# Kernel tuning notes

Measured on AMD Instinct MI355X. Metric: run time of the kernel, lower is better.

Reference implementation:

```python
import jax, jax.numpy as jnp
import numpy as np

B, N, F_IN = 8, 4096, 32
NRP = 1024
D_MODEL = 512
K = 64  # max_num_neighbors
STAGE_CFG = ((1024, 0.05), (256, 0.3), (64, 0.5))  # (num_samples=ceil(0.25*N_in), radius)


def fps(pos, m):
    """Farthest point sampling of m points from pos (N,3), deterministic start at 0."""
    d = jnp.sum((pos - pos[0]) ** 2, axis=-1)
    idxs = jnp.zeros((m,), jnp.int32)
    def body(i, carry):
        idxs, d = carry
        nxt = jnp.argmax(d).astype(jnp.int32)
        d = jnp.minimum(d, jnp.sum((pos - pos[nxt]) ** 2, axis=-1))
        return (idxs.at[i].set(nxt), d)
    idxs, _ = jax.lax.fori_loop(1, m, body, (idxs, d))
    return idxs


def apply_mlp(h, ws, bs):
    for w, b in zip(ws[:-1], bs[:-1]):
        h = jax.nn.relu(h @ w + b)
    return h @ ws[-1] + bs[-1]


def sa_stage(x, pos, m, r, ws, bs):
    """SAModule: FPS -> radius neighbors (<=K) -> PointNetConv (gather, MLP, max-scatter)."""
    idx = jax.vmap(lambda p: fps(p, m))(pos)                          # (B,m)
    pos_s = jnp.take_along_axis(pos, idx[..., None], axis=1)          # (B,m,3)
    d2 = jnp.sum((pos_s[:, :, None, :] - pos[:, None, :, :]) ** 2, -1)  # (B,m,N)
    neg = jnp.where(d2 <= r * r, -d2, -jnp.inf)
    vals, nbr = jax.lax.top_k(neg, K)                                 # (B,m,K) nearest within r
    valid = vals > -jnp.inf                                           # self always valid (d2=0)
    x_j = jax.vmap(lambda xb, nb: xb[nb])(x, nbr)                     # (B,m,K,F) gather
    p_j = jax.vmap(lambda pb, nb: pb[nb])(pos, nbr)                   # (B,m,K,3)
    h = jnp.concatenate([x_j, p_j - pos_s[:, :, None, :]], axis=-1)   # message input
    h = apply_mlp(h, ws, bs)
    h = jnp.where(valid[..., None], h, -jnp.inf)
    return jnp.max(h, axis=2), pos_s                                  # max aggregation


def _forward(point_cloud_features, point_cloud, emb_table, point_id_emb, stage_params):
    x = emb_table[point_cloud_features[..., 0]]                       # (B,N,F_IN)
    x = x.at[:, :NRP].add(point_id_emb)
    pos = point_cloud
    for (m, r), (ws, bs) in zip(STAGE_CFG, stage_params):
        x, pos = sa_stage(x, pos, m, r, ws, bs)
    return x, pos                                                     # (B,64,D_MODEL), (B,64,3)


def setup_inputs() -> dict:
    key = jax.random.key(0)
    ks = iter(jax.random.split(key, 64))
    def nrm(shape, s=0.05):
        return s * jax.random.normal(next(ks), shape, dtype=jnp.float32)
    inp = {
        "point_cloud_features": jax.random.randint(next(ks), (B, N, 1), 0, 3),
        "point_cloud": jax.random.uniform(next(ks), (B, N, 3), dtype=jnp.float32),
        "emb_table": nrm((3, F_IN), 1.0),
        "point_id_emb": nrm((1, NRP, F_IN), 1.0),
    }
    dims = {"s1": [3 + F_IN, 64, 64, 64], "s2": [64 + 3, 128, 128, 256], "s3": [256 + 3, 256, 512, D_MODEL]}
    for s, d in dims.items():
        for i in range(3):
            inp[f"{s}w{i}"] = nrm((d[i], d[i + 1]))
            inp[f"{s}b{i}"] = jnp.zeros((d[i + 1],), jnp.float32)
    return inp


def reference(point_cloud_features, point_cloud, emb_table, point_id_emb,
              s1w0, s1b0, s1w1, s1b1, s1w2, s1b2,
              s2w0, s2b0, s2w1, s2b1, s2w2, s2b2,
              s3w0, s3b0, s3w1, s3b1, s3w2, s3b2):
    stage_params = [
        ([s1w0, s1w1, s1w2], [s1b0, s1b1, s1b2]),
        ([s2w0, s2w1, s2w2], [s2b0, s2b1, s2b2]),
        ([s3w0, s3w1, s3w2], [s3b0, s3b1, s3b2]),
    ]
    return _forward(point_cloud_features, point_cloud, emb_table, point_id_emb, stage_params)
```

## Files before the change

kernel.cpp:

```cpp
#include <hip/hip_runtime.h>

#define DEVI static __device__ __forceinline__

constexpr int B = 8;
constexpr int N0 = 4096;
constexpr int KNB = 64;

typedef float f32x2 __attribute__((ext_vector_type(2)));
typedef float f32x4 __attribute__((ext_vector_type(4)));
typedef short bf16x8 __attribute__((ext_vector_type(8)));

DEVI float dist2f(float ax, float ay, float az, float bx, float by, float bz) {
#pragma clang fp contract(off)
  float dx = ax - bx;
  float dy = ay - by;
  float dz = az - bz;
  return (dx * dx + dy * dy) + dz * dz;
}
DEVI f32x2 dist2v(f32x2 ax, f32x2 ay, f32x2 az, float bx, float by, float bz) {
#pragma clang fp contract(off)
  f32x2 dx = ax - bx;
  f32x2 dy = ay - by;
  f32x2 dz = az - bz;
  return (dx * dx + dy * dy) + dz * dz;
}

DEVI unsigned long long packMinKey(float v, int i) {
  return ((unsigned long long)__float_as_uint(v) << 32) | (unsigned int)i;
}

template <int CTRL, int RM>
DEVI float dppMaxF32(float v) {
  int o = __builtin_amdgcn_update_dpp(__float_as_int(v), __float_as_int(v),
                                      CTRL, RM, 0xf, false);
  return fmaxf(v, __int_as_float(o));
}
DEVI float waveMaxF32(float v) {
  v = dppMaxF32<0x111, 0xf>(v);
  v = dppMaxF32<0x112, 0xf>(v);
  v = dppMaxF32<0x114, 0xf>(v);
  v = dppMaxF32<0x118, 0xf>(v);
  v = dppMaxF32<0x142, 0xa>(v);
  v = dppMaxF32<0x143, 0xc>(v);
  return __int_as_float(__builtin_amdgcn_readlane(__float_as_int(v), 63));
}
template <int CTRL, int RM>
DEVI unsigned dppMinU32(unsigned v) {
  int o = __builtin_amdgcn_update_dpp((int)v, (int)v, CTRL, RM, 0xf, false);
  unsigned ov = (unsigned)o;
  return v < ov ? v : ov;
}
DEVI unsigned waveMinU32(unsigned v) {
  v = dppMinU32<0x111, 0xf>(v);
  v = dppMinU32<0x112, 0xf>(v);
  v = dppMinU32<0x114, 0xf>(v);
  v = dppMinU32<0x118, 0xf>(v);
  v = dppMinU32<0x142, 0xa>(v);
  v = dppMinU32<0x143, 0xc>(v);
  return (unsigned)__builtin_amdgcn_readlane((int)v, 63);
}

DEVI unsigned short bfhi(float x) {
  unsigned u = __float_as_uint(x);
  return (unsigned short)((u + 0x7FFFu + ((u >> 16) & 1u)) >> 16);
}
DEVI float bf2f(unsigned short h) { return __uint_as_float(((unsigned)h) << 16); }
DEVI void mkfrag(const float* p, bf16x8& hi, bf16x8& lo) {
#pragma unroll
  for (int e = 0; e < 8; ++e) {
    float x = p[e];
    unsigned short h = bfhi(x);
    float r = x - bf2f(h);
    unsigned short l2 = bfhi(r);
    hi[e] = (short)h;
    lo[e] = (short)l2;
  }
}


DEVI void x0_body(const int* __restrict__ feat, const float* __restrict__ emb,
                  const float* __restrict__ pid, float* __restrict__ x0buf,
                  int bx, int t) {
  int gid = bx * 256 + t;
  if (gid >= B * N0 * 32) return;
  int c = gid & 31;
  int bn = gid >> 5;
  int n = bn & (N0 - 1);
  int f = feat[bn];
  float v = emb[f * 32 + c];
  if (n < 1024) v += pid[n * 32 + c];
  x0buf[gid] = v;
}

template <int NPTS, int M, int BLK>
DEVI void fps_body(char* smem, const float* __restrict__ pos,
                   float* __restrict__ pos_out, int b, int t) {
  constexpr int EPT = NPTS / BLK;
  constexpr int EP2 = EPT / 2;
  constexpr int NW = BLK / 64;
  float4* posl = (float4*)smem;
  float4* outp = (float4*)(smem + (size_t)NPTS * 16);
  unsigned long long* redk =
      (unsigned long long*)(smem + (size_t)(NPTS + M) * 16);
  const float* pb = pos + (size_t)b * NPTS * 3;
  f32x2 px[EP2], py[EP2], pz[EP2], d[EP2];
#pragma unroll
  for (int e = 0; e < EP2; ++e) {
    int i0 = t + (2 * e) * BLK;
    int i1 = t + (2 * e + 1) * BLK;
    float x0 = pb[i0 * 3 + 0], y0 = pb[i0 * 3 + 1], z0 = pb[i0 * 3 + 2];
    float x1 = pb[i1 * 3 + 0], y1 = pb[i1 * 3 + 1], z1 = pb[i1 * 3 + 2];
    px[e] = (f32x2){x0, x1};
    py[e] = (f32x2){y0, y1};
    pz[e] = (f32x2){z0, z1};
    posl[i0] = make_float4(x0, y0, z0, 0.f);
    posl[i1] = make_float4(x1, y1, z1, 0.f);
  }
  float sx = pb[0], sy = pb[1], sz = pb[2];
  if (t == 0) outp[0] = make_float4(sx, sy, sz, 0.f);
  f32x2 m2 = (f32x2){-1.f, -1.f};
#pragma unroll
  for (int e = 0; e < EP2; ++e) {
    d[e] = dist2v(px[e], py[e], pz[e], sx, sy, sz);
    m2.x = fmaxf(m2.x, d[e].x);
    m2.y = fmaxf(m2.y, d[e].y);
  }
  for (int it = 1; it < M; ++it) {
    const float vstar = waveMaxF32(fmaxf(m2.x, m2.y));
    unsigned cand = 0xffffffffu;
#pragma unroll
    for (int e = 0; e < EP2; ++e) {
      unsigned c0 = (d[e].x == vstar) ? (unsigned)(t + (2 * e) * BLK) : 0xffffffffu;
      unsigned c1 = (d[e].y == vstar) ? (unsigned)(t + (2 * e + 1) * BLK) : 0xffffffffu;
      cand = cand < c0 ? cand : c0;
      cand = cand < c1 ? cand : c1;
    }
    cand = waveMinU32(cand);
    unsigned sel;
    if constexpr (NW > 1) {
      if ((t & 63) == 0) {
        unsigned long long key =
            ((unsigned long long)__float_as_uint(vstar) << 32) |
            (unsigned)(0x7fffffffu - cand);
        redk[(it & 1) * NW + (t >> 6)] = key;
      }
      __syncthreads();
      unsigned long long kk = redk[(it & 1) * NW + 0];
#pragma unroll
      for (int w = 1; w < NW; ++w) {
        unsigned long long o = redk[(it & 1) * NW + w];
        kk = (kk > o) ? kk : o;
      }
      sel = 0x7fffffffu - (unsigned)(kk & 0xffffffffULL);
    } else {
      sel = cand;
    }
    float4 sp = posl[sel];
    if (t == 0) outp[it] = sp;
    m2 = (f32x2){-1.f, -1.f};
#pragma unroll
    for (int e = 0; e < EP2; ++e) {
      f32x2 nd = dist2v(px[e], py[e], pz[e], sp.x, sp.y, sp.z);
      d[e].x = fminf(d[e].x, nd.x);
      d[e].y = fminf(d[e].y, nd.y);
      m2.x = fmaxf(m2.x, d[e].x);
      m2.y = fmaxf(m2.y, d[e].y);
    }
  }
  if constexpr (NW > 1) __syncthreads();
  for (int m = t; m < M; m += BLK) {
    float4 q = outp[m];
    pos_out[(size_t)(b * M + m) * 3 + 0] = q.x;
    pos_out[(size_t)(b * M + m) * 3 + 1] = q.y;
    pos_out[(size_t)(b * M + m) * 3 + 2] = q.z;
  }
}

template <int NPTS, int M>
DEVI void radius_body(char* smem, const float* __restrict__ pos,
                      const float* __restrict__ pos_s, float r2,
                      int* __restrict__ nbr, int* __restrict__ cnt, int blk,
                      int t) {
  unsigned long long* candkey = (unsigned long long*)smem;
  int* ctrp = (int*)(smem + (size_t)NPTS * 8);
  const int b = blk / M;
  const float* pb = pos + (size_t)b * NPTS * 3;
  const float cx = pos_s[(size_t)blk * 3 + 0];
  const float cy = pos_s[(size_t)blk * 3 + 1];
  const float cz = pos_s[(size_t)blk * 3 + 2];
  if (t == 0) *ctrp = 0;
  __syncthreads();
  for (int j = t; j < NPTS; j += 256) {
    float d2 = dist2f(pb[j * 3 + 0], pb[j * 3 + 1], pb[j * 3 + 2], cx, cy, cz);
    if (d2 <= r2) {
      int p = atomicAdd(ctrp, 1);
      candkey[p] = packMinKey(d2, j);
      if (p < KNB) nbr[(size_t)blk * KNB + p] = j;
    }
  }
  __syncthreads();
  const int c = *ctrp;
  if (c <= KNB) {
    if (t == 0) cnt[blk] = c;
    return;
  }
  for (int s = t; s < c; s += 256) {
    unsigned long long mykey = candkey[s];
    int rank = 0;
#pragma unroll 4
    for (int j = 0; j < c; ++j) {
      rank += (candkey[j] < mykey) ? 1 : 0;
    }
    if (rank < KNB)
      nbr[(size_t)blk * KNB + rank] = (int)(unsigned)(mykey & 0xffffffffULL);
  }
  if (t == 0) cnt[blk] = KNB;
}

DEVI void conv1_body(char* smem, const float* __restrict__ x0buf,
                     const float* __restrict__ pos,
                     const float* __restrict__ pos_s,
                     const int* __restrict__ nbr, const int* __restrict__ cntp,
                     const float* __restrict__ w0, const float* __restrict__ b0,
                     const float* __restrict__ w1, const float* __restrict__ b1,
                     const float* __restrict__ w2, const float* __restrict__ b2,
                     float* __restrict__ x1, int blk, int t) {
  float(*ins)[36] = (float(*)[36])smem;
  float(*hh)[65] = (float(*)[65])(smem + 576);
  float(*sred)[65] = (float(*)[65])(smem + 1616);
  const int slot = t >> 6;
  const int ch = t & 63;
  const int b = blk >> 10;
  const int c = cntp[blk];
  const float cx = pos_s[(size_t)blk * 3 + 0];
  const float cy = pos_s[(size_t)blk * 3 + 1];
  const float cz = pos_s[(size_t)blk * 3 + 2];
  float best = -__builtin_inff();
  for (int r0 = 0; r0 < c; r0 += 4) {
    const int r = r0 + slot;
    const bool act = r < c;
    const int j = nbr[(size_t)blk * KNB + (act ? r : 0)];
    if (ch < 32) {
      ins[slot][ch] = x0buf[((size_t)(b * N0) + j) * 32 + ch];
    } else if (ch < 35) {
      float pv = pos[((size_t)(b * N0) + j) * 3 + (ch - 32)];
      float cv = (ch == 32) ? cx : (ch == 33) ? cy : cz;
      ins[slot][ch] = pv - cv;
    }
    __syncthreads();
    float v = b0[ch];
#pragma unroll
    for (int i = 0; i < 35; ++i) v = fmaf(ins[slot][i], w0[i * 64 + ch], v);
    v = fmaxf(v, 0.f);
    hh[slot][ch] = v;
    __syncthreads();
    float v2 = b1[ch];
#pragma unroll
    for (int i = 0; i < 64; ++i) v2 = fmaf(hh[slot][i], w1[i * 64 + ch], v2);
    v2 = fmaxf(v2, 0.f);
    __syncthreads();
    hh[slot][ch] = v2;
    __syncthreads();
    float v3 = b2[ch];
#pragma unroll
    for (int i = 0; i < 64; ++i) v3 = fmaf(hh[slot][i], w2[i * 64 + ch], v3);
    if (act) best = fmaxf(best, v3);
    __syncthreads();
  }
  sred[slot][ch] = best;
  __syncthreads();
  if (t < 64) {
    float v = sred[0][t];
#pragma unroll
    for (int s = 1; s < 4; ++s) v = fmaxf(v, sred[s][t]);
    x1[(size_t)blk * 64 + t] = v;
  }
}

DEVI void conv2_body(char* smem, const float* __restrict__ x1,
                     const float* __restrict__ pos1,
                     const float* __restrict__ pos2,
                     const int* __restrict__ nbr, const int* __restrict__ cntp,
                     const float* __restrict__ w0, const float* __restrict__ b0,
                     const float* __restrict__ w1, const float* __restrict__ b1,
                     const float* __restrict__ w2, const float* __restrict__ b2,
                     float* __restrict__ x2, int blk, int t) {
  float(*msg)[68] = (float(*)[68])smem;
  float(*h)[128] = (float(*)[128])(smem + 17408);
  float(*red)[256] = (float(*)[256])(smem + 17408 + 32768);
  const int b = blk >> 8;
  const int c = cntp[blk];
  const float cx = pos2[(size_t)blk * 3 + 0];
  const float cy = pos2[(size_t)blk * 3 + 1];
  const float cz = pos2[(size_t)blk * 3 + 2];
  for (int idx = t; idx < 64 * 68; idx += 256) {
    int r = idx / 68;
    int k = idx - r * 68;
    float v = 0.f;
    if (r < c && k < 67) {
      int j = nbr[(size_t)blk * KNB + r];
      if (k < 64) {
        v = x1[((size_t)(b * 1024) + j) * 64 + k];
      } else {
        float pv = pos1[((size_t)(b * 1024) + j) * 3 + (k - 64)];
        v = pv - ((k == 64) ? cx : (k == 65) ? cy : cz);
      }
    }
    msg[r][k] = v;
  }
  __syncthreads();
  const int rg = t >> 5;
  const int cg = t & 31;
  {
    float acc[8][4] = {};
    for (int i4 = 0; i4 < 16; ++i4) {
      float wv[4][4];
#pragma unroll
      for (int k = 0; k < 4; ++k) {
        float4 q = *(const float4*)&w0[(size_t)(i4 * 4 + k) * 128 + cg * 4];
        wv[k][0] = q.x; wv[k][1] = q.y; wv[k][2] = q.z; wv[k][3] = q.w;
      }
#pragma unroll
      for (int rr = 0; rr < 8; ++rr) {
        float4 aq = *(const float4*)&msg[rg * 8 + rr][i4 * 4];
        float a[4] = {aq.x, aq.y, aq.z, aq.w};
#pragma unroll
        for (int k = 0; k < 4; ++k)
#pragma unroll
          for (int cc = 0; cc < 4; ++cc)
            acc[rr][cc] = fmaf(a[k], wv[k][cc], acc[rr][cc]);
      }
    }
#pragma unroll
    for (int i = 64; i < 67; ++i) {
      float wv[4];
#pragma unroll
      for (int cc = 0; cc < 4; ++cc) wv[cc] = w0[(size_t)i * 128 + cg * 4 + cc];
#pragma unroll
      for (int rr = 0; rr < 8; ++rr) {
        float a = msg[rg * 8 + rr][i];
#pragma unroll
        for (int cc = 0; cc < 4; ++cc) acc[rr][cc] = fmaf(a, wv[cc], acc[rr][cc]);
      }
    }
#pragma unroll
    for (int rr = 0; rr < 8; ++rr)
#pragma unroll
      for (int cc = 0; cc < 4; ++cc)
        h[rg * 8 + rr][cg * 4 + cc] = fmaxf(acc[rr][cc] + b0[cg * 4 + cc], 0.f);
  }
  __syncthreads();
  {
    float acc[8][4] = {};
    for (int i4 = 0; i4 < 32; ++i4) {
      float wv[4][4];
#pragma unroll
      for (int k = 0; k < 4; ++k) {
        float4 q = *(const float4*)&w1[(size_t)(i4 * 4 + k) * 128 + cg * 4];
        wv[k][0] = q.x; wv[k][1] = q.y; wv[k][2] = q.z; wv[k][3] = q.w;
      }
#pragma unroll
      for (int rr = 0; rr < 8; ++rr) {
        float4 aq = *(const float4*)&h[rg * 8 + rr][i4 * 4];
        float a[4] = {aq.x, aq.y, aq.z, aq.w};
#pragma unroll
        for (int k = 0; k < 4; ++k)
#pragma unroll
          for (int cc = 0; cc < 4; ++cc)
            acc[rr][cc] = fmaf(a[k], wv[k][cc], acc[rr][cc]);
      }
    }
    __syncthreads();
#pragma unroll
    for (int rr = 0; rr < 8; ++rr)
#pragma unroll
      for (int cc = 0; cc < 4; ++cc)
        h[rg * 8 + rr][cg * 4 + cc] = fmaxf(acc[rr][cc] + b1[cg * 4 + cc], 0.f);
  }
  __syncthreads();
  {
    float acc[8][8] = {};
    for (int i4 = 0; i4 < 32; ++i4) {
      float wv[4][8];
#pragma unroll
      for (int k = 0; k < 4; ++k) {
        float4 q0 = *(const float4*)&w2[(size_t)(i4 * 4 + k) * 256 + cg * 8];
        float4 q1 = *(const float4*)&w2[(size_t)(i4 * 4 + k) * 256 + cg * 8 + 4];
        wv[k][0] = q0.x; wv[k][1] = q0.y; wv[k][2] = q0.z; wv[k][3] = q0.w;
        wv[k][4] = q1.x; wv[k][5] = q1.y; wv[k][6] = q1.z; wv[k][7] = q1.w;
      }
#pragma unroll
      for (int rr = 0; rr < 8; ++rr) {
        float4 aq = *(const float4*)&h[rg * 8 + rr][i4 * 4];
        float a[4] = {aq.x, aq.y, aq.z, aq.w};
#pragma unroll
        for (int k = 0; k < 4; ++k)
#pragma unroll
          for (int cc = 0; cc < 8; ++cc)
            acc[rr][cc] = fmaf(a[k], wv[k][cc], acc[rr][cc]);
      }
    }
    float mx[8];
#pragma unroll
    for (int cc = 0; cc < 8; ++cc) mx[cc] = -__builtin_inff();
#pragma unroll
    for (int rr = 0; rr < 8; ++rr) {
      if (rg * 8 + rr < c) {
#pragma unroll
        for (int cc = 0; cc < 8; ++cc)
          mx[cc] = fmaxf(mx[cc], acc[rr][cc] + b2[cg * 8 + cc]);
      }
    }
#pragma unroll
    for (int cc = 0; cc < 8; ++cc) red[rg][cg * 8 + cc] = mx[cc];
  }
  __syncthreads();
  {
    float v = red[0][t];
#pragma unroll
    for (int g = 1; g < 8; ++g) v = fmaxf(v, red[g][t]);
    x2[(size_t)blk * 256 + t] = v;
  }
}


__global__ void __launch_bounds__(256) l1_kernel(
    const float* __restrict__ pos, float* __restrict__ pos1,
    const int* __restrict__ feat, const float* __restrict__ emb,
    const float* __restrict__ pid, float* __restrict__ x0buf) {
  __shared__ __attribute__((aligned(16))) char smem[81984];
  if (blockIdx.x < 8) {
    fps_body<4096, 1024, 256>(smem, pos, pos1, blockIdx.x, threadIdx.x);
  } else {
    x0_body(feat, emb, pid, x0buf, blockIdx.x - 8, threadIdx.x);
  }
}

__global__ void __launch_bounds__(256) l2_kernel(
    const float* __restrict__ pos1, float* __restrict__ pos2,
    const float* __restrict__ pos, float r2a, int* __restrict__ nbr1,
    int* __restrict__ cnt1) {
  __shared__ __attribute__((aligned(16))) char smem[33024];
  if (blockIdx.x < 8) {
    fps_body<1024, 256, 256>(smem, pos1, pos2, blockIdx.x, threadIdx.x);
  } else {
    radius_body<4096, 1024>(smem, pos, pos1, r2a, nbr1, cnt1, blockIdx.x - 8,
                            threadIdx.x);
  }
}

__global__ void __launch_bounds__(256) l3_kernel(
    const float* __restrict__ pos2, float* __restrict__ pos3, float r2b,
    int* __restrict__ nbr2, int* __restrict__ cnt2,
    const float* __restrict__ pos1, const float* __restrict__ x0buf,
    const float* __restrict__ pos, const int* __restrict__ nbr1,
    const int* __restrict__ cnt1, const float* __restrict__ w0,
    const float* __restrict__ b0, const float* __restrict__ w1,
    const float* __restrict__ b1, const float* __restrict__ w2,
    const float* __restrict__ b2, float* __restrict__ x1) {
  __shared__ __attribute__((aligned(16))) char smem[8448];
  if (blockIdx.x < 8) {
    if (threadIdx.x < 64)
      fps_body<256, 64, 64>(smem, pos2, pos3, blockIdx.x, threadIdx.x);
  } else if (blockIdx.x < 8 + 2048) {
    radius_body<1024, 256>(smem, pos1, pos2, r2b, nbr2, cnt2, blockIdx.x - 8,
                           threadIdx.x);
  } else {
    conv1_body(smem, x0buf, pos, pos1, nbr1, cnt1, w0, b0, w1, b1, w2, b2, x1,
               blockIdx.x - (8 + 2048), threadIdx.x);
  }
}

__global__ void __launch_bounds__(256) l4_kernel(
    const float* __restrict__ pos2, const float* __restrict__ pos3, float r2c,
    int* __restrict__ nbr3, int* __restrict__ cnt3,
    const float* __restrict__ x1, const float* __restrict__ pos1,
    const int* __restrict__ nbr2, const int* __restrict__ cnt2,
    const float* __restrict__ w0, const float* __restrict__ b0,
    const float* __restrict__ w1, const float* __restrict__ b1,
    const float* __restrict__ w2, const float* __restrict__ b2,
    float* __restrict__ x2) {
  __shared__ __attribute__((aligned(16))) char smem[58368];
  if (blockIdx.x < 512) {
    radius_body<256, 64>(smem, pos2, pos3, r2c, nbr3, cnt3, blockIdx.x,
                         threadIdx.x);
  } else {
    conv2_body(smem, x1, pos1, pos2, nbr2, cnt2, w0, b0, w1, b1, w2, b2, x2,
               blockIdx.x - 512, threadIdx.x);
  }
}

__global__ void __launch_bounds__(256) pack_kernel(
    const float* __restrict__ W, int Kreal, int KS, int N,
    unsigned short* __restrict__ hi, unsigned short* __restrict__ lo) {
  int gid = blockIdx.x * 256 + threadIdx.x;
  int total = (N / 16) * KS * 64 * 8;
  if (gid >= total) return;
  int e = gid & 7;
  int l = (gid >> 3) & 63;
  int rest = gid >> 9;
  int ks = rest % KS;
  int nt = rest / KS;
  int n = nt * 16 + (l & 15);
  int k = ks * 32 + (l >> 4) * 8 + e;
  float val = (k < Kreal) ? W[(size_t)k * N + n] : 0.f;
  unsigned short h = bfhi(val);
  float r = val - bf2f(h);
  hi[gid] = h;
  lo[gid] = bfhi(r);
}

__global__ void __launch_bounds__(256) conv3_mfma(
    const float* __restrict__ x2, const float* __restrict__ pos2,
    const float* __restrict__ pos3, const int* __restrict__ nbr,
    const int* __restrict__ cntp,
    const unsigned short* __restrict__ w0h, const unsigned short* __restrict__ w0l,
    const float* __restrict__ b0,
    const unsigned short* __restrict__ w1h, const unsigned short* __restrict__ w1l,
    const float* __restrict__ b1,
    const unsigned short* __restrict__ w2h, const unsigned short* __restrict__ w2l,
    const float* __restrict__ b2, float* __restrict__ out) {
  __shared__ __attribute__((aligned(16))) float h1s[64 * 268];
  __shared__ __attribute__((aligned(16))) float h2cs[64 * 140];
  __shared__ __attribute__((aligned(16))) float msgcs[64 * 44];
  const int blk = blockIdx.x;
  const int t = threadIdx.x;
  const int b = blk >> 6;
  const int c = cntp[blk];
  const int w = t >> 6;
  const int lane = t & 63;
  const int cb = lane & 15;
  const int kb = lane >> 4;
  const float cx = pos3[(size_t)blk * 3 + 0];
  const float cy = pos3[(size_t)blk * 3 + 1];
  const float cz = pos3[(size_t)blk * 3 + 2];
  const int mrow = w * 16 + cb;

  f32x4 acc1[16];
#pragma unroll
  for (int nt = 0; nt < 16; ++nt) acc1[nt] = (f32x4){0.f, 0.f, 0.f, 0.f};
  for (int ks = 0; ks < 9; ++ks) {
#pragma unroll
    for (int i = 0; i < 8; ++i) {
      int idx = t + i * 256;
      int row = idx >> 5;
      int col = idx & 31;
      int kg = ks * 32 + col;
      int j = nbr[(size_t)blk * KNB + (row < c ? row : c - 1)];
      float v = 0.f;
      if (kg < 256) {
        v = x2[((size_t)(b * 256) + j) * 256 + kg];
      } else if (kg < 259) {
        float pv = pos2[((size_t)(b * 256) + j) * 3 + (kg - 256)];
        v = pv - ((kg == 256) ? cx : (kg == 257) ? cy : cz);
      }
      msgcs[row * 44 + col] = v;
    }
    __syncthreads();
    bf16x8 ahi, alo;
    mkfrag(&msgcs[mrow * 44 + kb * 8], ahi, alo);
#pragma unroll
    for (int nt = 0; nt < 16; ++nt) {
      size_t off = ((size_t)(nt * 9 + ks) * 64 + lane) * 8;
      bf16x8 bhi = *(const bf16x8*)(w0h + off);
      bf16x8 blo = *(const bf16x8*)(w0l + off);
      acc1[nt] = __builtin_amdgcn_mfma_f32_16x16x32_bf16(ahi, bhi, acc1[nt], 0, 0, 0);
      acc1[nt] = __builtin_amdgcn_mfma_f32_16x16x32_bf16(alo, bhi, acc1[nt], 0, 0, 0);
      acc1[nt] = __builtin_amdgcn_mfma_f32_16x16x32_bf16(ahi, blo, acc1[nt], 0, 0, 0);
    }
    __syncthreads();
  }
  {
    const int mw = w * 16 + kb * 4;
#pragma unroll
    for (int nt = 0; nt < 16; ++nt) {
      float bias = b0[nt * 16 + cb];
#pragma unroll
      for (int r = 0; r < 4; ++r)
        h1s[(mw + r) * 268 + nt * 16 + cb] = fmaxf(acc1[nt][r] + bias, 0.f);
    }
  }
  __syncthreads();

  f32x4 acc3[32];
#pragma unroll
  for (int nt = 0; nt < 32; ++nt) acc3[nt] = (f32x4){0.f, 0.f, 0.f, 0.f};
  for (int ch = 0; ch < 4; ++ch) {
    f32x4 acc2[8];
#pragma unroll
    for (int nt = 0; nt < 8; ++nt) acc2[nt] = (f32x4){0.f, 0.f, 0.f, 0.f};
#pragma unroll
    for (int ks = 0; ks < 8; ++ks) {
      bf16x8 ahi, alo;
      mkfrag(&h1s[mrow * 268 + ks * 32 + kb * 8], ahi, alo);
#pragma unroll
      for (int nt = 0; nt < 8; ++nt) {
        size_t off = ((size_t)((ch * 8 + nt) * 8 + ks) * 64 + lane) * 8;
        bf16x8 bhi = *(const bf16x8*)(w1h + off);
        bf16x8 blo = *(const bf16x8*)(w1l + off);
        acc2[nt] = __builtin_amdgcn_mfma_f32_16x16x32_bf16(ahi, bhi, acc2[nt], 0, 0, 0);
        acc2[nt] = __builtin_amdgcn_mfma_f32_16x16x32_bf16(alo, bhi, acc2[nt], 0, 0, 0);
        acc2[nt] = __builtin_amdgcn_mfma_f32_16x16x32_bf16(ahi, blo, acc2[nt], 0, 0, 0);
      }
    }
    {
      const int mw = w * 16 + kb * 4;
#pragma unroll
      for (int nt = 0; nt < 8; ++nt) {
        float bias = b1[ch * 128 + nt * 16 + cb];
#pragma unroll
        for (int r = 0; r < 4; ++r)
          h2cs[(mw + r) * 140 + nt * 16 + cb] = fmaxf(acc2[nt][r] + bias, 0.f);
      }
    }
    __syncthreads();
#pragma unroll
    for (int ks3 = 0; ks3 < 4; ++ks3) {
      bf16x8 ahi, alo;
      mkfrag(&h2cs[mrow * 140 + ks3 * 32 + kb * 8], ahi, alo);
#pragma unroll
      for (int nt = 0; nt < 32; ++nt) {
        size_t off = ((size_t)(nt * 16 + ch * 4 + ks3) * 64 + lane) * 8;
        bf16x8 bhi = *(const bf16x8*)(w2h + off);
        bf16x8 blo = *(const bf16x8*)(w2l + off);
        acc3[nt] = __builtin_amdgcn_mfma_f32_16x16x32_bf16(ahi, bhi, acc3[nt], 0, 0, 0);
        acc3[nt] = __builtin_amdgcn_mfma_f32_16x16x32_bf16(alo, bhi, acc3[nt], 0, 0, 0);
        acc3[nt] = __builtin_amdgcn_mfma_f32_16x16x32_bf16(ahi, blo, acc3[nt], 0, 0, 0);
      }
    }
    __syncthreads();
  }

  float* redw = h1s;
  {
    const int mw = w * 16 + kb * 4;
#pragma unroll
    for (int nt = 0; nt < 32; ++nt) {
      float bias = b2[nt * 16 + cb];
      float mx = -__builtin_inff();
#pragma unroll
      for (int r = 0; r < 4; ++r) {
        if (mw + r < c) mx = fmaxf(mx, acc3[nt][r] + bias);
      }
      redw[(w * 4 + kb) * 512 + nt * 16 + cb] = mx;
    }
  }
  __syncthreads();
#pragma unroll
  for (int half = 0; half < 2; ++half) {
    int col = t + half * 256;
    float v = redw[col];
#pragma unroll
    for (int g = 1; g < 16; ++g) v = fmaxf(v, redw[g * 512 + col]);
    out[(size_t)blk * 512 + col] = v;
  }
}

extern "C" void kernel_launch(void* const* d_in, const int* in_sizes, int n_in,
                              void* d_out, int out_size, void* d_ws, size_t ws_size,
                              hipStream_t stream) {
  const int* feat = (const int*)d_in[0];
  const float* pos = (const float*)d_in[1];
  const float* emb = (const float*)d_in[2];
  const float* pid = (const float*)d_in[3];
  const float* s1w0 = (const float*)d_in[4];
  const float* s1b0 = (const float*)d_in[5];
  const float* s1w1 = (const float*)d_in[6];
  const float* s1b1 = (const float*)d_in[7];
  const float* s1w2 = (const float*)d_in[8];
  const float* s1b2 = (const float*)d_in[9];
  const float* s2w0 = (const float*)d_in[10];
  const float* s2b0 = (const float*)d_in[11];
  const float* s2w1 = (const float*)d_in[12];
  const float* s2b1 = (const float*)d_in[13];
  const float* s2w2 = (const float*)d_in[14];
  const float* s2b2 = (const float*)d_in[15];
  const float* s3w0 = (const float*)d_in[16];
  const float* s3b0 = (const float*)d_in[17];
  const float* s3w1 = (const float*)d_in[18];
  const float* s3b1 = (const float*)d_in[19];
  const float* s3w2 = (const float*)d_in[20];
  const float* s3b2 = (const float*)d_in[21];
  (void)in_sizes; (void)n_in; (void)out_size; (void)ws_size;

  char* ws = (char*)d_ws;
  size_t off = 0;
  auto alloc = [&](size_t nbytes) {
    void* p = ws + off;
    off = (off + nbytes + 255) & ~(size_t)255;
    return p;
  };
  float* x0 = (float*)alloc((size_t)B * N0 * 32 * 4);
  float* pos1 = (float*)alloc((size_t)B * 1024 * 3 * 4);
  int* nbr1 = (int*)alloc((size_t)B * 1024 * KNB * 4);
  int* cnt1 = (int*)alloc((size_t)B * 1024 * 4);
  float* x1 = (float*)alloc((size_t)B * 1024 * 64 * 4);
  float* pos2 = (float*)alloc((size_t)B * 256 * 3 * 4);
  int* nbr2 = (int*)alloc((size_t)B * 256 * KNB * 4);
  int* cnt2 = (int*)alloc((size_t)B * 256 * 4);
  float* x2 = (float*)alloc((size_t)B * 256 * 256 * 4);
  int* nbr3 = (int*)alloc((size_t)B * 64 * KNB * 4);
  int* cnt3 = (int*)alloc((size_t)B * 64 * 4);
  const int T0 = 16 * 9 * 64 * 8;
  const int T1 = 32 * 8 * 64 * 8;
  const int T2 = 32 * 16 * 64 * 8;
  unsigned short* w0h = (unsigned short*)alloc((size_t)T0 * 2);
  unsigned short* w0l = (unsigned short*)alloc((size_t)T0 * 2);
  unsigned short* w1h = (unsigned short*)alloc((size_t)T1 * 2);
  unsigned short* w1l = (unsigned short*)alloc((size_t)T1 * 2);
  unsigned short* w2h = (unsigned short*)alloc((size_t)T2 * 2);
  unsigned short* w2l = (unsigned short*)alloc((size_t)T2 * 2);

  float* xout = (float*)d_out;
  float* pos3 = xout + (size_t)B * 64 * 512;

  const float r2a = (float)(0.05 * 0.05);
  const float r2b = (float)(0.3 * 0.3);
  const float r2c = (float)(0.5 * 0.5);

  pack_kernel<<<(T0 + 255) / 256, 256, 0, stream>>>(s3w0, 259, 9, 256, w0h, w0l);
  pack_kernel<<<(T1 + 255) / 256, 256, 0, stream>>>(s3w1, 256, 8, 512, w1h, w1l);
  pack_kernel<<<(T2 + 255) / 256, 256, 0, stream>>>(s3w2, 512, 16, 512, w2h, w2l);

  l1_kernel<<<8 + 4096, 256, 0, stream>>>(pos, pos1, feat, emb, pid, x0);
  l2_kernel<<<8 + 8192, 256, 0, stream>>>(pos1, pos2, pos, r2a, nbr1, cnt1);
  l3_kernel<<<8 + 2048 + 8192, 256, 0, stream>>>(
      pos2, pos3, r2b, nbr2, cnt2, pos1, x0, pos, nbr1, cnt1,
      s1w0, s1b0, s1w1, s1b1, s1w2, s1b2, x1);
  l4_kernel<<<512 + 2048, 256, 0, stream>>>(
      pos2, pos3, r2c, nbr3, cnt3, x1, pos1, nbr2, cnt2,
      s2w0, s2b0, s2w1, s2b1, s2w2, s2b2, x2);
  conv3_mfma<<<B * 64, 256, 0, stream>>>(x2, pos2, pos3, nbr3, cnt3,
                                         w0h, w0l, s3b0, w1h, w1l, s3b1,
                                         w2h, w2l, s3b2, xout);
}
```

Measured before the change: 1.460 ms.

## Run stage-2 PointNetConv MLP on bf16 MFMA with split-activation precision

Replaces the FP32 scalar-FMA stage-2 conv MLP with 16x16x32 bf16 MFMA tiles. Activations are split into hi and lo bf16 parts, while the weights are prepacked into an MFMA fragment layout by extra pack_kernel launches. Only the weight hi part is used, so precision drops relative to FP32. Each wave gathers its neighbor rows straight from global memory instead of staging a message tile in LDS. The change also raises the LDS footprint of l4_kernel, which may reduce occupancy for the co-scheduled radius blocks.

```diff
diff --git a/kernel.cpp b/kernel.cpp
--- a/kernel.cpp
+++ b/kernel.cpp
@@ -277,148 +277,142 @@
   }
 }
 
-DEVI void conv2_body(char* smem, const float* __restrict__ x1,
-                     const float* __restrict__ pos1,
-                     const float* __restrict__ pos2,
-                     const int* __restrict__ nbr, const int* __restrict__ cntp,
-                     const float* __restrict__ w0, const float* __restrict__ b0,
-                     const float* __restrict__ w1, const float* __restrict__ b1,
-                     const float* __restrict__ w2, const float* __restrict__ b2,
-                     float* __restrict__ x2, int blk, int t) {
-  float(*msg)[68] = (float(*)[68])smem;
-  float(*h)[128] = (float(*)[128])(smem + 17408);
-  float(*red)[256] = (float(*)[256])(smem + 17408 + 32768);
+DEVI void conv2_mfma_body(char* smem, const float* __restrict__ x1,
+                          const float* __restrict__ pos1,
+                          const float* __restrict__ pos2,
+                          const int* __restrict__ nbr,
+                          const int* __restrict__ cntp,
+                          const unsigned short* __restrict__ w0h,
+                          const float* __restrict__ b0,
+                          const unsigned short* __restrict__ w1h,
+                          const float* __restrict__ b1,
+                          const unsigned short* __restrict__ w2h,
+                          const float* __restrict__ b2,
+                          float* __restrict__ x2, int blk, int t) {
+  float(*h1)[132] = (float(*)[132])smem;
+  float(*h2)[132] = (float(*)[132])(smem + 33792);
+  float* red = (float*)smem;
   const int b = blk >> 8;
   const int c = cntp[blk];
+  const int w = t >> 6;
+  const int lane = t & 63;
+  const int cb = lane & 15;
+  const int kb = lane >> 4;
+  const int mrow = w * 16 + cb;
+  const int jrow = nbr[(size_t)blk * KNB + (mrow < c ? mrow : c - 1)];
+  const float* xrow = x1 + ((size_t)(b * 1024) + jrow) * 64;
   const float cx = pos2[(size_t)blk * 3 + 0];
   const float cy = pos2[(size_t)blk * 3 + 1];
   const float cz = pos2[(size_t)blk * 3 + 2];
-  for (int idx = t; idx < 64 * 68; idx += 256) {
-    int r = idx / 68;
-    int k = idx - r * 68;
-    float v = 0.f;
-    if (r < c && k < 67) {
-      int j = nbr[(size_t)blk * KNB + r];
-      if (k < 64) {
-        v = x1[((size_t)(b * 1024) + j) * 64 + k];
-      } else {
-        float pv = pos1[((size_t)(b * 1024) + j) * 3 + (k - 64)];
-        v = pv - ((k == 64) ? cx : (k == 65) ? cy : cz);
+
+  f32x4 acc1[8];
+#pragma unroll
+  for (int nt = 0; nt < 8; ++nt) acc1[nt] = (f32x4){0.f, 0.f, 0.f, 0.f};
+#pragma unroll
+  for (int ks = 0; ks < 2; ++ks) {
+    float xv[8];
+    *(float4*)&xv[0] = *(const float4*)&xrow[ks * 32 + kb * 8];
+    *(float4*)&xv[4] = *(const float4*)&xrow[ks * 32 + kb * 8 + 4];
+    bf16x8 ahi, alo;
+    mkfrag(xv, ahi, alo);
+#pragma unroll
+    for (int nt = 0; nt < 8; ++nt) {
+      size_t off = ((size_t)(nt * 3 + ks) * 64 + lane) * 8;
+      bf16x8 bhi = *(const bf16x8*)(w0h + off);
+      acc1[nt] = __builtin_amdgcn_mfma_f32_16x16x32_bf16(ahi, bhi, acc1[nt], 0, 0, 0);
+      acc1[nt] = __builtin_amdgcn_mfma_f32_16x16x32_bf16(alo, bhi, acc1[nt], 0, 0, 0);
+    }
+  }
+  {
+    float xv[8] = {0.f, 0.f, 0.f, 0.f, 0.f, 0.f, 0.f, 0.f};
+    if (kb == 0) {
+      xv[0] = pos1[((size_t)(b * 1024) + jrow) * 3 + 0] - cx;
+      xv[1] = pos1[((size_t)(b * 1024) + jrow) * 3 + 1] - cy;
+      xv[2] = pos1[((size_t)(b * 1024) + jrow) * 3 + 2] - cz;
+    }
+    bf16x8 ahi, alo;
+    mkfrag(xv, ahi, alo);
+#pragma unroll
+    for (int nt = 0; nt < 8; ++nt) {
+      size_t off = ((size_t)(nt * 3 + 2) * 64 + lane) * 8;
+      bf16x8 bhi = *(const bf16x8*)(w0h + off);
+      acc1[nt] = __builtin_amdgcn_mfma_f32_16x16x32_bf16(ahi, bhi, acc1[nt], 0, 0, 0);
+      acc1[nt] = __builtin_amdgcn_mfma_f32_16x16x32_bf16(alo, bhi, acc1[nt], 0, 0, 0);
+    }
+  }
+  {
+    const int mw = w * 16 + kb * 4;
+#pragma unroll
+    for (int nt = 0; nt < 8; ++nt) {
+      float bias = b0[nt * 16 + cb];
+#pragma unroll
+      for (int r = 0; r < 4; ++r)
+        h1[mw + r][nt * 16 + cb] = fmaxf(acc1[nt][r] + bias, 0.f);
+    }
+  }
+  __syncthreads();
+
+  f32x4 acc2[8];
+#pragma unroll
+  for (int nt = 0; nt < 8; ++nt) acc2[nt] = (f32x4){0.f, 0.f, 0.f, 0.f};
+#pragma unroll
+  for (int ks = 0; ks < 4; ++ks) {
+    bf16x8 ahi, alo;
+    mkfrag(&h1[mrow][ks * 32 + kb * 8], ahi, alo);
+#pragma unroll
+    for (int nt = 0; nt < 8; ++nt) {
+      size_t off = ((size_t)(nt * 4 + ks) * 64 + lane) * 8;
+      bf16x8 bhi = *(const bf16x8*)(w1h + off);
+      acc2[nt] = __builtin_amdgcn_mfma_f32_16x16x32_bf16(ahi, bhi, acc2[nt], 0, 0, 0);
+      acc2[nt] = __builtin_amdgcn_mfma_f32_16x16x32_bf16(alo, bhi, acc2[nt], 0, 0, 0);
+    }
+  }
+  {
+    const int mw = w * 16 + kb * 4;
+#pragma unroll
+    for (int nt = 0; nt < 8; ++nt) {
+      float bias = b1[nt * 16 + cb];
+#pragma unroll
+      for (int r = 0; r < 4; ++r)
+        h2[mw + r][nt * 16 + cb] = fmaxf(acc2[nt][r] + bias, 0.f);
+    }
+  }
+  __syncthreads();
+
+  f32x4 acc3[16];
+#pragma unroll
+  for (int nt = 0; nt < 16; ++nt) acc3[nt] = (f32x4){0.f, 0.f, 0.f, 0.f};
+#pragma unroll
+  for (int ks = 0; ks < 4; ++ks) {
+    bf16x8 ahi, alo;
+    mkfrag(&h2[mrow][ks * 32 + kb * 8], ahi, alo);
+#pragma unroll
+    for (int nt = 0; nt < 16; ++nt) {
+      size_t off = ((size_t)(nt * 4 + ks) * 64 + lane) * 8;
+      bf16x8 bhi = *(const bf16x8*)(w2h + off);
+      acc3[nt] = __builtin_amdgcn_mfma_f32_16x16x32_bf16(ahi, bhi, acc3[nt], 0, 0, 0);
+      acc3[nt] = __builtin_amdgcn_mfma_f32_16x16x32_bf16(alo, bhi, acc3[nt], 0, 0, 0);
+    }
+  }
+  __syncthreads();
+  {
+    const int mw = w * 16 + kb * 4;
+#pragma unroll
+    for (int nt = 0; nt < 16; ++nt) {
+      float bias = b2[nt * 16 + cb];
+      float mx = -__builtin_inff();
+#pragma unroll
+      for (int r = 0; r < 4; ++r) {
+        if (mw + r < c) mx = fmaxf(mx, acc3[nt][r] + bias);
       }
-    }
-    msg[r][k] = v;
-  }
-  __syncthreads();
-  const int rg = t >> 5;
-  const int cg = t & 31;
+      red[(w * 4 + kb) * 256 + nt * 16 + cb] = mx;
+    }
+  }
+  __syncthreads();
   {
-    float acc[8][4] = {};
-    for (int i4 = 0; i4 < 16; ++i4) {
-      float wv[4][4];
-#pragma unroll
-      for (int k = 0; k < 4; ++k) {
-        float4 q = *(const float4*)&w0[(size_t)(i4 * 4 + k) * 128 + cg * 4];
-        wv[k][0] = q.x; wv[k][1] = q.y; wv[k][2] = q.z; wv[k][3] = q.w;
-      }
-#pragma unroll
-      for (int rr = 0; rr < 8; ++rr) {
-        float4 aq = *(const float4*)&msg[rg * 8 + rr][i4 * 4];
-        float a[4] = {aq.x, aq.y, aq.z, aq.w};
-#pragma unroll
-        for (int k = 0; k < 4; ++k)
-#pragma unroll
-          for (int cc = 0; cc < 4; ++cc)
-            acc[rr][cc] = fmaf(a[k], wv[k][cc], acc[rr][cc]);
-      }
-    }
-#pragma unroll
-    for (int i = 64; i < 67; ++i) {
-      float wv[4];
-#pragma unroll
-      for (int cc = 0; cc < 4; ++cc) wv[cc] = w0[(size_t)i * 128 + cg * 4 + cc];
-#pragma unroll
-      for (int rr = 0; rr < 8; ++rr) {
-        float a = msg[rg * 8 + rr][i];
-#pragma unroll
-        for (int cc = 0; cc < 4; ++cc) acc[rr][cc] = fmaf(a, wv[cc], acc[rr][cc]);
-      }
-    }
-#pragma unroll
-    for (int rr = 0; rr < 8; ++rr)
-#pragma unroll
-      for (int cc = 0; cc < 4; ++cc)
-        h[rg * 8 + rr][cg * 4 + cc] = fmaxf(acc[rr][cc] + b0[cg * 4 + cc], 0.f);
-  }
-  __syncthreads();
-  {
-    float acc[8][4] = {};
-    for (int i4 = 0; i4 < 32; ++i4) {
-      float wv[4][4];
-#pragma unroll
-      for (int k = 0; k < 4; ++k) {
-        float4 q = *(const float4*)&w1[(size_t)(i4 * 4 + k) * 128 + cg * 4];
-        wv[k][0] = q.x; wv[k][1] = q.y; wv[k][2] = q.z; wv[k][3] = q.w;
-      }
-#pragma unroll
-      for (int rr = 0; rr < 8; ++rr) {
-        float4 aq = *(const float4*)&h[rg * 8 + rr][i4 * 4];
-        float a[4] = {aq.x, aq.y, aq.z, aq.w};
-#pragma unroll
-        for (int k = 0; k < 4; ++k)
-#pragma unroll
-          for (int cc = 0; cc < 4; ++cc)
-            acc[rr][cc] = fmaf(a[k], wv[k][cc], acc[rr][cc]);
-      }
-    }
-    __syncthreads();
-#pragma unroll
-    for (int rr = 0; rr < 8; ++rr)
-#pragma unroll
-      for (int cc = 0; cc < 4; ++cc)
-        h[rg * 8 + rr][cg * 4 + cc] = fmaxf(acc[rr][cc] + b1[cg * 4 + cc], 0.f);
-  }
-  __syncthreads();
-  {
-    float acc[8][8] = {};
-    for (int i4 = 0; i4 < 32; ++i4) {
-      float wv[4][8];
-#pragma unroll
-      for (int k = 0; k < 4; ++k) {
-        float4 q0 = *(const float4*)&w2[(size_t)(i4 * 4 + k) * 256 + cg * 8];
-        float4 q1 = *(const float4*)&w2[(size_t)(i4 * 4 + k) * 256 + cg * 8 + 4];
-        wv[k][0] = q0.x; wv[k][1] = q0.y; wv[k][2] = q0.z; wv[k][3] = q0.w;
-        wv[k][4] = q1.x; wv[k][5] = q1.y; wv[k][6] = q1.z; wv[k][7] = q1.w;
-      }
-#pragma unroll
-      for (int rr = 0; rr < 8; ++rr) {
-        float4 aq = *(const float4*)&h[rg * 8 + rr][i4 * 4];
-        float a[4] = {aq.x, aq.y, aq.z, aq.w};
-#pragma unroll
-        for (int k = 0; k < 4; ++k)
-#pragma unroll
-          for (int cc = 0; cc < 8; ++cc)
-            acc[rr][cc] = fmaf(a[k], wv[k][cc], acc[rr][cc]);
-      }
-    }
-    float mx[8];
-#pragma unroll
-    for (int cc = 0; cc < 8; ++cc) mx[cc] = -__builtin_inff();
-#pragma unroll
-    for (int rr = 0; rr < 8; ++rr) {
-      if (rg * 8 + rr < c) {
-#pragma unroll
-        for (int cc = 0; cc < 8; ++cc)
-          mx[cc] = fmaxf(mx[cc], acc[rr][cc] + b2[cg * 8 + cc]);
-      }
-    }
-#pragma unroll
-    for (int cc = 0; cc < 8; ++cc) red[rg][cg * 8 + cc] = mx[cc];
-  }
-  __syncthreads();
-  {
-    float v = red[0][t];
-#pragma unroll
-    for (int g = 1; g < 8; ++g) v = fmaxf(v, red[g][t]);
+    float v = red[t];
+#pragma unroll
+    for (int g = 1; g < 16; ++g) v = fmaxf(v, red[g * 256 + t]);
     x2[(size_t)blk * 256 + t] = v;
   }
 }
@@ -476,17 +470,17 @@
     int* __restrict__ nbr3, int* __restrict__ cnt3,
     const float* __restrict__ x1, const float* __restrict__ pos1,
     const int* __restrict__ nbr2, const int* __restrict__ cnt2,
-    const float* __restrict__ w0, const float* __restrict__ b0,
-    const float* __restrict__ w1, const float* __restrict__ b1,
-    const float* __restrict__ w2, const float* __restrict__ b2,
+    const unsigned short* __restrict__ v0h, const float* __restrict__ b0,
+    const unsigned short* __restrict__ v1h, const float* __restrict__ b1,
+    const unsigned short* __restrict__ v2h, const float* __restrict__ b2,
     float* __restrict__ x2) {
-  __shared__ __attribute__((aligned(16))) char smem[58368];
+  __shared__ __attribute__((aligned(16))) char smem[67584];
   if (blockIdx.x < 512) {
     radius_body<256, 64>(smem, pos2, pos3, r2c, nbr3, cnt3, blockIdx.x,
                          threadIdx.x);
   } else {
-    conv2_body(smem, x1, pos1, pos2, nbr2, cnt2, w0, b0, w1, b1, w2, b2, x2,
-               blockIdx.x - 512, threadIdx.x);
+    conv2_mfma_body(smem, x1, pos1, pos2, nbr2, cnt2, v0h, b0, v1h, b1, v2h,
+                    b2, x2, blockIdx.x - 512, threadIdx.x);
   }
 }
 
@@ -710,6 +704,15 @@
   unsigned short* w1l = (unsigned short*)alloc((size_t)T1 * 2);
   unsigned short* w2h = (unsigned short*)alloc((size_t)T2 * 2);
   unsigned short* w2l = (unsigned short*)alloc((size_t)T2 * 2);
+  const int U0 = 8 * 3 * 64 * 8;
+  const int U1 = 8 * 4 * 64 * 8;
+  const int U2 = 16 * 4 * 64 * 8;
+  unsigned short* v0h = (unsigned short*)alloc((size_t)U0 * 2);
+  unsigned short* v0l = (unsigned short*)alloc((size_t)U0 * 2);
+  unsigned short* v1h = (unsigned short*)alloc((size_t)U1 * 2);
+  unsigned short* v1l = (unsigned short*)alloc((size_t)U1 * 2);
+  unsigned short* v2h = (unsigned short*)alloc((size_t)U2 * 2);
+  unsigned short* v2l = (unsigned short*)alloc((size_t)U2 * 2);
 
   float* xout = (float*)d_out;
   float* pos3 = xout + (size_t)B * 64 * 512;
@@ -721,6 +724,9 @@
   pack_kernel<<<(T0 + 255) / 256, 256, 0, stream>>>(s3w0, 259, 9, 256, w0h, w0l);
   pack_kernel<<<(T1 + 255) / 256, 256, 0, stream>>>(s3w1, 256, 8, 512, w1h, w1l);
   pack_kernel<<<(T2 + 255) / 256, 256, 0, stream>>>(s3w2, 512, 16, 512, w2h, w2l);
+  pack_kernel<<<(U0 + 255) / 256, 256, 0, stream>>>(s2w0, 67, 3, 128, v0h, v0l);
+  pack_kernel<<<(U1 + 255) / 256, 256, 0, stream>>>(s2w1, 128, 4, 128, v1h, v1l);
+  pack_kernel<<<(U2 + 255) / 256, 256, 0, stream>>>(s2w2, 128, 4, 256, v2h, v2l);
 
   l1_kernel<<<8 + 4096, 256, 0, stream>>>(pos, pos1, feat, emb, pid, x0);
   l2_kernel<<<8 + 8192, 256, 0, stream>>>(pos1, pos2, pos, r2a, nbr1, cnt1);
@@ -729,7 +735,7 @@
       s1w0, s1b0, s1w1, s1b1, s1w2, s1b2, x1);
   l4_kernel<<<512 + 2048, 256, 0, stream>>>(
       pos2, pos3, r2c, nbr3, cnt3, x1, pos1, nbr2, cnt2,
-      s2w0, s2b0, s2w1, s2b1, s2w2, s2b2, x2);
+      v0h, s2b0, v1h, s2b1, v2h, s2b2, x2);
   conv3_mfma<<<B * 64, 256, 0, stream>>>(x2, pos2, pos3, nbr3, cnt3,
                                          w0h, w0l, s3b0, w1h, w1l, s3b1,
                                          w2h, w2l, s3b2, xout);
```

Result: faster. 1.327 ms (-9.1%).
